# Performance work log

Hardware: AMD Instinct MI355X
Metric: run time of the kernel (lower is better)

Reference implementation:

```python
import jax, jax.numpy as jnp
import numpy as np

NUM_HEADS = 8
D_MODEL = 512
HEAD_DIM = D_MODEL // NUM_HEADS


def _conv1x1(x, W, b):
    # Conv1d(kernel_size=1): x [B, Cin, N], W [Cout, Cin], b [Cout] -> [B, Cout, N]
    return jnp.einsum('oi,bin->bon', W, x) + b[None, :, None]


def setup_inputs() -> dict:
    key = jax.random.key(0)
    ks = jax.random.split(key, 12)
    B, D, N, Mlen = 4, D_MODEL, 2048, 2048
    inp = {
        'query': jax.random.normal(ks[0], (B, D, N), dtype=jnp.float32),
        'key':   jax.random.normal(ks[1], (B, D, Mlen), dtype=jnp.float32),
        'value': jax.random.normal(ks[2], (B, D, Mlen), dtype=jnp.float32),
        'M':     jnp.ones((B, N, Mlen), dtype=jnp.int32),
    }
    scale = 0.02
    inp['Wq'] = jax.random.normal(ks[3], (D, D), dtype=jnp.float32) * scale
    inp['bq'] = jnp.zeros((D,), dtype=jnp.float32)
    inp['Wk'] = jax.random.normal(ks[4], (D, D), dtype=jnp.float32) * scale
    inp['bk'] = jnp.zeros((D,), dtype=jnp.float32)
    inp['Wv'] = jax.random.normal(ks[5], (D, D), dtype=jnp.float32) * scale
    inp['bv'] = jnp.zeros((D,), dtype=jnp.float32)
    inp['Wm'] = jax.random.normal(ks[6], (D, D), dtype=jnp.float32) * scale
    inp['bm'] = jnp.zeros((D,), dtype=jnp.float32)
    return inp


def reference(query, key, value, M, Wq, bq, Wk, bk, Wv, bv, Wm, bm):
    B = query.shape[0]
    # 1x1-conv projections, then channel split as [head_dim, heads] (matches torch .view)
    q = _conv1x1(query, Wq, bq).reshape(B, HEAD_DIM, NUM_HEADS, -1)  # [B, d, h, N]
    k = _conv1x1(key,   Wk, bk).reshape(B, HEAD_DIM, NUM_HEADS, -1)  # [B, d, h, M]
    v = _conv1x1(value, Wv, bv).reshape(B, HEAD_DIM, NUM_HEADS, -1)  # [B, d, h, M]
    scores = jnp.einsum('bdhn,bdhm->bhnm', q, k) / jnp.sqrt(jnp.float32(HEAD_DIM))
    # mask: positions with M==0 are disallowed -> fill with -finfo.max
    bad = (1 - M)[:, None, :, :].astype(bool)  # [B, 1, N, M], broadcasts over heads
    scores = jnp.where(bad, -jnp.finfo(scores.dtype).max, scores)
    prob = jax.nn.softmax(scores, axis=-1)  # [B, h, N, M]
    x = jnp.einsum('bhnm,bdhm->bdhn', prob, v)  # [B, d, h, N]
    out = _conv1x1(x.reshape(B, HEAD_DIM * NUM_HEADS, -1), Wm, bm)  # [B, D, N]
    return out
```

## Files before the change

### kernel.cpp

```cpp
#include <hip/hip_runtime.h>

typedef __attribute__((ext_vector_type(8))) short s8v;
typedef __attribute__((ext_vector_type(4))) float f4v;
typedef _Float16 h4 __attribute__((ext_vector_type(4)));
typedef unsigned short u16;
typedef unsigned long long u64;

#define DM 512
#define NH 8
#define HD 64
#define BB 4
#define NN 2048

__device__ __forceinline__ float bf2f(u16 x){ return __uint_as_float(((unsigned)x)<<16); }
__device__ __forceinline__ u16 f2bf(float f){
  unsigned u = __float_as_uint(f);
  u += 0x7FFFu + ((u>>16)&1u);
  return (u16)(u>>16);
}
__device__ __forceinline__ void gl2lds16(const u16* g, u16* l){
  __builtin_amdgcn_global_load_lds((__attribute__((address_space(1))) void*)(g),
                                   (__attribute__((address_space(3))) void*)(l), 16, 0, 0);
}

__global__ __launch_bounds__(256) void k_maskpack(const int* M, u64* bits){
  int tid = threadIdx.x;
  int wv = tid>>6, lane = tid&63;
  size_t w0 = (size_t)blockIdx.x*64 + wv*16;
  #pragma unroll
  for (int it=0; it<16; it++){
    int v = M[(w0+it)*64 + lane];
    u64 bal = __ballot(v == 1);
    if (lane == 0) bits[w0+it] = bal;
  }
}

__global__ void k_prep(const float* Wq, const float* bq, const float* Wk, const float* bk,
                       const float* Wv, const float* bv, const float* Wm,
                       u16* Wp, u16* Wmp, float* bp,
                       const u64* bits, u64* allw){
  int blk = blockIdx.x, tid = threadIdx.x;
  if (blk < 1536){
    int t = blk >> 9, op = blk & 511;
    int srow = ((op & 63) << 3) | (op >> 6);
    const float* W = (t==0) ? Wq : ((t==1) ? Wk : Wv);
    for (int j = tid; j < 512; j += 256)
      Wp[((size_t)t*512 + op)*512 + j] = f2bf(W[(size_t)srow*512 + j]);
  } else if (blk < 2048){
    int o = blk - 1536;
    for (int c = tid; c < 512; c += 256){
      int scol = ((c & 63) << 3) | (c >> 6);
      Wmp[(size_t)o*512 + c] = f2bf(Wm[(size_t)o*512 + scol]);
    }
  } else if (blk == 2048){
    for (int idx = tid; idx < 1536; idx += 256){
      int t = idx >> 9, op = idx & 511;
      const float* bs = (t==0) ? bq : ((t==1) ? bk : bv);
      int srow = ((op & 63) << 3) | (op >> 6);
      bp[idx] = bs[srow];
    }
  } else {
    __shared__ u64 red[256];
    int bnt = blk - 2049;
    int mt = tid & 31, rg = tid >> 5;
    const u64* base = bits + (size_t)bnt*64*32;
    u64 v = ~0ull;
    #pragma unroll
    for (int j=0;j<8;j++) v &= base[(size_t)(rg*8+j)*32 + mt];
    red[tid] = v;
    __syncthreads();
    if (tid < 32){
      u64 a = red[tid];
      #pragma unroll
      for (int g2=1; g2<8; g2++) a &= red[g2*32 + tid];
      allw[(size_t)bnt*32 + tid] = a;
    }
  }
}

__global__ __launch_bounds__(256) void k_transpose(const float* q, const float* k, const float* v, u16* XT){
  __shared__ u16 T[64*72];
  int blk = blockIdx.x, tid = threadIdx.x;
  int rt = blk & 31; blk >>= 5;
  int it = blk & 7;  blk >>= 3;
  int b  = blk & 3;  int t = blk >> 2;
  const float* src = (t==0) ? q : ((t==1) ? k : v);
  src += (size_t)b*DM*NN;
  int i0 = it*64, r0 = rt*64;
  int il = tid>>4, rj = (tid&15)*4;
  #pragma unroll
  for (int p=0;p<4;p++){
    int i = il + p*16;
    float4 vv = *(const float4*)&src[(size_t)(i0+i)*NN + r0 + rj];
    float fv[4] = {vv.x, vv.y, vv.z, vv.w};
    #pragma unroll
    for (int qq=0;qq<4;qq++){
      int r = rj + qq;
      int sr = ((r&3)<<4) | (r>>2);
      T[sr*72 + i] = f2bf(fv[qq]);
    }
  }
  __syncthreads();
  u16* dst = XT + ((size_t)(t*4+b)*NN)*DM;
  int rl = tid>>3, ib = (tid&7)*8;
  #pragma unroll
  for (int p=0;p<2;p++){
    int r = rl + p*32;
    int sr = ((r&3)<<4) | (r>>2);
    s8v vv = *(s8v*)&T[sr*72 + ib];
    *(s8v*)&dst[(size_t)(r0+r)*DM + i0 + ib] = vv;
  }
}

__global__ __launch_bounds__(256) void k_proj(const u16* XT, const u16* Wp, const float* bp,
                                              u16* P, u16* VT){
  __shared__ u16 Al[128*32];
  __shared__ u16 Bl[128*32];
  __shared__ u16 S[128*72];
  int blk = blockIdx.x, tid = threadIdx.x;
  int nt = blk & 3; int mt = blk >> 2;
  int tb = mt >> 4;
  int t  = tb >> 2, b = tb & 3;
  int r0 = (mt & 15)*128, o0 = nt*128;
  const u16* Abase = XT + ((size_t)tb*NN + r0)*DM;
  const u16* Bbase = Wp + ((size_t)t*512 + o0)*DM;

  int w = tid>>6, L = tid&63, li = L&15, lq = L>>4;
  int wr = w>>1, wc = w&1;
  int srow = tid>>2;
  int g8   = ((tid&3) ^ ((tid>>3)&3))*8;
  u16* AldsW = &Al[((tid&192))*8];
  u16* BldsW = &Bl[((tid&192))*8];
  int sw = (li>>1)&3;

  f4v acc[4][4];
  #pragma unroll
  for (int a=0;a<4;a++)
    #pragma unroll
    for (int c2=0;c2<4;c2++) acc[a][c2] = (f4v){0.f,0.f,0.f,0.f};

  for (int kk=0; kk<16; kk++){
    int k0 = kk*32;
    __syncthreads();
    #pragma unroll
    for (int c=0;c<2;c++){
      gl2lds16(&Abase[(size_t)(srow + c*64)*DM + k0 + g8], AldsW + c*2048);
      gl2lds16(&Bbase[(size_t)(srow + c*64)*DM + k0 + g8], BldsW + c*2048);
    }
    __syncthreads();
    s8v af[4], bfr[4];
    #pragma unroll
    for (int a=0;a<4;a++){
      int r = wr*64 + a*16 + li;
      af[a] = *(s8v*)&Al[r*32 + ((lq ^ sw))*8];
    }
    #pragma unroll
    for (int c2=0;c2<4;c2++){
      int r = wc*64 + c2*16 + li;
      bfr[c2] = *(s8v*)&Bl[r*32 + ((lq ^ sw))*8];
    }
    #pragma unroll
    for (int a=0;a<4;a++)
      #pragma unroll
      for (int c2=0;c2<4;c2++)
        acc[a][c2] = __builtin_amdgcn_mfma_f32_16x16x32_bf16(af[a], bfr[c2], acc[a][c2], 0, 0, 0);
  }

  if (t < 2){
    float scale = (t==0) ? 0.125f : 1.0f;
    #pragma unroll
    for (int p=0;p<2;p++){
      if (wc == p){
        #pragma unroll
        for (int c2=0;c2<4;c2++){
          int cl = c2*16 + li;
          float bias = bp[t*512 + o0 + p*64 + cl];
          #pragma unroll
          for (int a=0;a<4;a++)
            #pragma unroll
            for (int ri=0;ri<4;ri++)
              S[(wr*64 + a*16 + lq*4 + ri)*72 + cl] = f2bf((acc[a][c2][ri] + bias)*scale);
        }
      }
      __syncthreads();
      int row = tid>>1, cb = (tid&1)*32;
      int hh = (o0>>6) + p;
      u16* Pb = P + (((size_t)tb*NH + hh)*NN + r0 + row)*HD + cb;
      #pragma unroll
      for (int c=0;c<4;c++){
        s8v vv = *(s8v*)&S[row*72 + cb + c*8];
        *(s8v*)&Pb[c*8] = vv;
      }
      __syncthreads();
    }
  } else {
    #pragma unroll
    for (int p=0;p<2;p++){
      if (wc == p){
        #pragma unroll
        for (int c2=0;c2<4;c2++){
          int cl = c2*16 + li;
          float bias = bp[2*512 + o0 + p*64 + cl];
          #pragma unroll
          for (int a=0;a<4;a++)
            #pragma unroll
            for (int ri=0;ri<4;ri++){
              _Float16 hh = (_Float16)(acc[a][c2][ri] + bias);
              S[(wr*64 + a*16 + lq*4 + ri)*72 + cl] = *(const u16*)&hh;
            }
        }
      }
      __syncthreads();
      int hh = (o0>>6) + p;
      u16* Vb = VT + (((size_t)b*NH + hh)*NN + r0)*HD;
      #pragma unroll
      for (int it2=0; it2<4; it2++){
        int c = tid + it2*256;
        int mb = c >> 7;
        int co = c & 127;
        int d  = co >> 1;
        int m8 = (co & 1)*8;
        u16 tmp[8];
        #pragma unroll
        for (int j=0;j<8;j++) tmp[j] = S[(mb*16 + m8 + j)*72 + d];
        *(s8v*)&Vb[(size_t)mb*1024 + d*16 + m8] = *(s8v*)&tmp[0];
      }
      __syncthreads();
    }
  }
}

__global__ __launch_bounds__(256) void k_flash(const u16* Pq, const u16* VT, const u64* bits,
                                               const u64* allw, u16* Xout){
  __shared__ __align__(16) char smem[18432 + 1024];
  float* Red = (float*)smem;
  float* lsb = (float*)(smem + 18432);

  int blk = blockIdx.x, tid = threadIdx.x;
  int bh = blk & 31; int nt = blk >> 5;
  int b = bh >> 3;
  int n0 = nt*64;
  const size_t TSZ = (size_t)BB*NH*NN*HD;
  const u16* Qb = Pq + ((size_t)bh*NN + n0)*HD;
  const u16* Kb = Pq + TSZ + (size_t)bh*NN*HD;
  const u16* Vb = VT + (size_t)bh*NN*HD;
  const u64* awp = allw + ((size_t)b*32 + nt)*32;

  int w = tid>>6, L = tid&63, li = L&15, lq = L>>4;

  s8v Qf[4][2];
  #pragma unroll
  for (int j=0;j<4;j++)
    #pragma unroll
    for (int h2=0;h2<2;h2++)
      Qf[j][h2] = *(const s8v*)&Qb[(size_t)(j*16+li)*HD + h2*32 + lq*8];

  f4v O[4][4];
  #pragma unroll
  for (int j2=0;j2<4;j2++)
    #pragma unroll
    for (int j=0;j<4;j++) O[j2][j] = (f4v){0.f,0.f,0.f,0.f};
  float ls[4] = {0.f,0.f,0.f,0.f};

  const u16* Krow = Kb + (size_t)(w*16 + li)*HD + lq*8;
  const u16* Vrow = Vb + (size_t)w*1024 + li*16 + lq*4;

  s8v cK0 = *(const s8v*)&Krow[0];
  s8v cK1 = *(const s8v*)&Krow[32];
  h4 cV[4];
  #pragma unroll
  for (int j2=0;j2<4;j2++) cV[j2] = *(const h4*)&Vrow[j2*256];

  for (int mt=0; mt<32; mt++){
    size_t noff = (size_t)((mt+1)&31)*4096;
    s8v nK0 = *(const s8v*)&Krow[noff];
    s8v nK1 = *(const s8v*)&Krow[noff + 32];
    h4 nV[4];
    #pragma unroll
    for (int j2=0;j2<4;j2++) nV[j2] = *(const h4*)&Vrow[noff + j2*256];

    u64 aw = awp[mt];
    bool fast = (aw == ~0ull);

    f4v S[4];
    #pragma unroll
    for (int j=0;j<4;j++){
      f4v c = (f4v){0.f,0.f,0.f,0.f};
      c = __builtin_amdgcn_mfma_f32_16x16x32_bf16(cK0, Qf[j][0], c, 0, 0, 0);
      c = __builtin_amdgcn_mfma_f32_16x16x32_bf16(cK1, Qf[j][1], c, 0, 0, 0);
      S[j] = c;
    }

    h4 Pf[4];
    if (fast){
      #pragma unroll
      for (int j=0;j<4;j++){
        float e0 = __expf(S[j][0]), e1 = __expf(S[j][1]);
        float e2 = __expf(S[j][2]), e3 = __expf(S[j][3]);
        ls[j] += (e0+e1)+(e2+e3);
        Pf[j][0] = (_Float16)e0; Pf[j][1] = (_Float16)e1;
        Pf[j][2] = (_Float16)e2; Pf[j][3] = (_Float16)e3;
      }
    } else {
      int mbit = w*16 + lq*4;
      #pragma unroll
      for (int j=0;j<4;j++){
        u64 mw = bits[((size_t)b*NN + n0 + j*16 + li)*32 + mt];
        float e[4];
        #pragma unroll
        for (int r=0;r<4;r++){
          float ev = __expf(S[j][r]);
          e[r] = ((mw>>(mbit+r)) & 1ull) ? ev : 0.f;
          Pf[j][r] = (_Float16)e[r];
        }
        ls[j] += (e[0]+e[1])+(e[2]+e[3]);
      }
    }

    #pragma unroll
    for (int j2=0;j2<4;j2++)
      #pragma unroll
      for (int j=0;j<4;j++)
        O[j2][j] = __builtin_amdgcn_mfma_f32_16x16x16f16(cV[j2], Pf[j], O[j2][j], 0, 0, 0);

    cK0 = nK0; cK1 = nK1;
    #pragma unroll
    for (int j2=0;j2<4;j2++) cV[j2] = nV[j2];
  }

  #pragma unroll
  for (int j=0;j<4;j++){
    float r = ls[j];
    r += __shfl_xor(r, 16); r += __shfl_xor(r, 32);
    ls[j] = r;
  }
  if (lq == 0){
    #pragma unroll
    for (int j=0;j<4;j++) lsb[w*64 + j*16 + li] = ls[j];
  }
  __syncthreads();

  #pragma unroll
  for (int ph=0; ph<4; ph++){
    if (w == ph){
      #pragma unroll
      for (int j=0;j<4;j++)
        #pragma unroll
        for (int j2=0;j2<4;j2++){
          f4v* p = (f4v*)&Red[(j*16+li)*68 + j2*16 + lq*4];
          if (ph == 0) *p = O[j2][j];
          else { f4v t = *p; t += O[j2][j]; *p = t; }
        }
    }
    __syncthreads();
  }

  int n = tid>>2, d0 = (tid&3)*16;
  float s = lsb[n] + lsb[64+n] + lsb[128+n] + lsb[192+n];
  float inv = (s > 0.f) ? 1.0f/s : 0.f;
  int h = bh & 7;
  u16* Xo = Xout + ((size_t)b*NN + n0 + n)*DM + h*HD + d0;
  u16 tmp[16];
  #pragma unroll
  for (int e2=0;e2<4;e2++){
    f4v vv = *(f4v*)&Red[n*68 + d0 + e2*4];
    #pragma unroll
    for (int q2=0;q2<4;q2++) tmp[e2*4+q2] = f2bf(vv[q2]*inv);
  }
  *(s8v*)&Xo[0] = *(s8v*)&tmp[0];
  *(s8v*)&Xo[8] = *(s8v*)&tmp[8];
}

__global__ __launch_bounds__(256) void k_out(const u16* Wmp, const u16* Xout, const float* bm, float* out){
  __shared__ u16 Al[64*32];
  __shared__ u16 Bl[128*32];
  int blk = blockIdx.x, tid = threadIdx.x;
  int nt = blk & 15; blk >>= 4;
  int ot = blk & 7;  int b = blk >> 3;
  int o0 = ot*64, n0 = nt*128;
  const u16* Abase = Wmp + (size_t)o0*DM;
  const u16* Bbase = Xout + ((size_t)b*NN + n0)*DM;

  int w = tid>>6, L = tid&63, li = L&15, lq = L>>4;
  int wo = w&1, wn = w>>1;
  int srow = tid>>2;
  int g8   = ((tid&3) ^ ((tid>>3)&3))*8;
  u16* AldsW = &Al[((tid&192))*8];
  u16* BldsW = &Bl[((tid&192))*8];
  int sw = (li>>1)&3;

  f4v acc[2][4];
  #pragma unroll
  for (int a=0;a<2;a++)
    #pragma unroll
    for (int c2=0;c2<4;c2++) acc[a][c2] = (f4v){0.f,0.f,0.f,0.f};

  for (int kk=0; kk<16; kk++){
    int k0 = kk*32;
    __syncthreads();
    gl2lds16(&Abase[(size_t)srow*DM + k0 + g8], AldsW);
    #pragma unroll
    for (int c=0;c<2;c++)
      gl2lds16(&Bbase[(size_t)(srow + c*64)*DM + k0 + g8], BldsW + c*2048);
    __syncthreads();
    s8v af[2], bfr[4];
    #pragma unroll
    for (int a=0;a<2;a++){
      int r = wo*32 + a*16 + li;
      af[a] = *(s8v*)&Al[r*32 + ((lq ^ sw))*8];
    }
    #pragma unroll
    for (int c2=0;c2<4;c2++){
      int r = wn*64 + c2*16 + li;
      bfr[c2] = *(s8v*)&Bl[r*32 + ((lq ^ sw))*8];
    }
    #pragma unroll
    for (int a=0;a<2;a++)
      #pragma unroll
      for (int c2=0;c2<4;c2++)
        acc[a][c2] = __builtin_amdgcn_mfma_f32_16x16x32_bf16(af[a], bfr[c2], acc[a][c2], 0, 0, 0);
  }

  #pragma unroll
  for (int a=0;a<2;a++){
    #pragma unroll
    for (int ri=0;ri<4;ri++){
      int o = o0 + wo*32 + a*16 + lq*4 + ri;
      float bias = bm[o];
      float* ob = out + ((size_t)b*DM + o)*NN + n0 + wn*64;
      #pragma unroll
      for (int c2=0;c2<4;c2++)
        ob[c2*16 + li] = acc[a][c2][ri] + bias;
    }
  }
}

extern "C" void kernel_launch(void* const* d_in, const int* in_sizes, int n_in,
                              void* d_out, int out_size, void* d_ws, size_t ws_size,
                              hipStream_t stream){
  const float* q  = (const float*)d_in[0];
  const float* k  = (const float*)d_in[1];
  const float* v  = (const float*)d_in[2];
  const int*   M  = (const int*)d_in[3];
  const float* Wq = (const float*)d_in[4];
  const float* bq = (const float*)d_in[5];
  const float* Wk = (const float*)d_in[6];
  const float* bk = (const float*)d_in[7];
  const float* Wv = (const float*)d_in[8];
  const float* bv = (const float*)d_in[9];
  const float* Wm = (const float*)d_in[10];
  const float* bm = (const float*)d_in[11];

  char* ws = (char*)d_ws;
  u16*   XT   = (u16*)(ws + 0);
  u16*   P    = (u16*)(ws + 25165824);
  u16*   VT   = (u16*)(ws + 41943040);
  u16*   Wp   = (u16*)(ws + 50331648);
  u16*   Wmp  = (u16*)(ws + 51904512);
  float* bp   = (float*)(ws + 52428800);
  u64*   bits = (u64*)(ws + 52434944);
  u16*   Xout = (u16*)(ws + 54532096);
  u64*   allw = (u64*)(ws + 62920704);
  float* out  = (float*)d_out;

  k_maskpack<<<4096, 256, 0, stream>>>(M, bits);
  k_prep<<<2177, 256, 0, stream>>>(Wq, bq, Wk, bk, Wv, bv, Wm, Wp, Wmp, bp, bits, allw);
  k_transpose<<<3072, 256, 0, stream>>>(q, k, v, XT);
  k_proj<<<768, 256, 0, stream>>>(XT, Wp, bp, P, VT);
  k_flash<<<1024, 256, 0, stream>>>(P, VT, bits, allw, Xout);
  k_out<<<512, 256, 0, stream>>>(Wmp, Xout, bm, out);
}
```

Baseline: 277.3 us.

## Use 16x16x32 f16 MFMA for PV with repacked V layout and exp2

Processes two 64-key tiles per iteration in the flash kernel so the P·V product can use the wider 16x16x32 f16 MFMA instead of 16x16x16. The V projection output is repacked so each lane loads 8 contiguous halves per MFMA operand. The Q scale now folds in log2(e) so softmax uses native exp2. It also adds s_setprio around the MFMA blocks and reorders the projection block index mapping. V loads are no longer prefetched one iteration ahead, which may expose memory latency, and the extra score tiles raise register pressure.

```diff
diff --git a/kernel.cpp b/kernel.cpp
--- a/kernel.cpp
+++ b/kernel.cpp
@@ -2,7 +2,7 @@
 
 typedef __attribute__((ext_vector_type(8))) short s8v;
 typedef __attribute__((ext_vector_type(4))) float f4v;
-typedef _Float16 h4 __attribute__((ext_vector_type(4)));
+typedef _Float16 h8 __attribute__((ext_vector_type(8)));
 typedef unsigned short u16;
 typedef unsigned long long u64;
 
@@ -11,6 +11,9 @@
 #define HD 64
 #define BB 4
 #define NN 2048
+
+extern "C" __device__ float __ocml_native_exp2_f32(float);
+__device__ __forceinline__ float fexp2(float x){ return __ocml_native_exp2_f32(x); }
 
 __device__ __forceinline__ float bf2f(u16 x){ return __uint_as_float(((unsigned)x)<<16); }
 __device__ __forceinline__ u16 f2bf(float f){
@@ -118,7 +121,7 @@
   __shared__ u16 Bl[128*32];
   __shared__ u16 S[128*72];
   int blk = blockIdx.x, tid = threadIdx.x;
-  int nt = blk & 3; int mt = blk >> 2;
+  int nt = blk / 192; int mt = blk % 192;
   int tb = mt >> 4;
   int t  = tb >> 2, b = tb & 3;
   int r0 = (mt & 15)*128, o0 = nt*128;
@@ -167,7 +170,7 @@
   }
 
   if (t < 2){
-    float scale = (t==0) ? 0.125f : 1.0f;
+    float scale = (t==0) ? 0.18033688f : 1.0f;
     #pragma unroll
     for (int p=0;p<2;p++){
       if (wc == p){
@@ -194,6 +197,7 @@
       __syncthreads();
     }
   } else {
+    int mp = mt & 15;
     #pragma unroll
     for (int p=0;p<2;p++){
       if (wc == p){
@@ -212,18 +216,20 @@
       }
       __syncthreads();
       int hh = (o0>>6) + p;
-      u16* Vb = VT + (((size_t)b*NH + hh)*NN + r0)*HD;
+      u16* Vbw = VT + ((size_t)(b*NH + hh)*16 + mp)*8192;
       #pragma unroll
       for (int it2=0; it2<4; it2++){
         int c = tid + it2*256;
-        int mb = c >> 7;
-        int co = c & 127;
-        int d  = co >> 1;
-        int m8 = (co & 1)*8;
+        int w2  = c >> 8;
+        int d   = (c >> 2) & 63;
+        int lq2 = c & 3;
         u16 tmp[8];
         #pragma unroll
-        for (int j=0;j<8;j++) tmp[j] = S[(mb*16 + m8 + j)*72 + d];
-        *(s8v*)&Vb[(size_t)mb*1024 + d*16 + m8] = *(s8v*)&tmp[0];
+        for (int t2=0;t2<8;t2++){
+          int ml = ((t2>>2)<<6) + w2*16 + lq2*4 + (t2&3);
+          tmp[t2] = S[ml*72 + d];
+        }
+        *(s8v*)&Vbw[(size_t)w2*2048 + d*32 + lq2*8] = *(s8v*)&tmp[0];
       }
       __syncthreads();
     }
@@ -263,53 +269,56 @@
   float ls[4] = {0.f,0.f,0.f,0.f};
 
   const u16* Krow = Kb + (size_t)(w*16 + li)*HD + lq*8;
-  const u16* Vrow = Vb + (size_t)w*1024 + li*16 + lq*4;
-
-  s8v cK0 = *(const s8v*)&Krow[0];
-  s8v cK1 = *(const s8v*)&Krow[32];
-  h4 cV[4];
-  #pragma unroll
-  for (int j2=0;j2<4;j2++) cV[j2] = *(const h4*)&Vrow[j2*256];
-
-  for (int mt=0; mt<32; mt++){
-    size_t noff = (size_t)((mt+1)&31)*4096;
-    s8v nK0 = *(const s8v*)&Krow[noff];
-    s8v nK1 = *(const s8v*)&Krow[noff + 32];
-    h4 nV[4];
-    #pragma unroll
-    for (int j2=0;j2<4;j2++) nV[j2] = *(const h4*)&Vrow[noff + j2*256];
-
-    u64 aw = awp[mt];
-    bool fast = (aw == ~0ull);
-
+  const u16* Vrow = Vb + (size_t)w*2048 + li*32 + lq*8;
+
+  s8v cKA0 = *(const s8v*)&Krow[0];
+  s8v cKA1 = *(const s8v*)&Krow[32];
+  s8v cKB0 = *(const s8v*)&Krow[4096];
+  s8v cKB1 = *(const s8v*)&Krow[4128];
+
+  int mbit = w*16 + lq*4;
+
+  for (int mp=0; mp<16; mp++){
+    size_t noff = (size_t)((mp+1)&15)*8192;
+    s8v nKA0 = *(const s8v*)&Krow[noff];
+    s8v nKA1 = *(const s8v*)&Krow[noff + 32];
+    s8v nKB0 = *(const s8v*)&Krow[noff + 4096];
+    s8v nKB1 = *(const s8v*)&Krow[noff + 4128];
+    size_t voff = (size_t)mp*8192;
+    h8 cV[4];
+    #pragma unroll
+    for (int j2=0;j2<4;j2++) cV[j2] = *(const h8*)&Vrow[voff + j2*512];
+
+    u64 awA = awp[2*mp], awB = awp[2*mp+1];
+    h8 Pf[4];
     f4v S[4];
+
+    __builtin_amdgcn_s_setprio(1);
     #pragma unroll
     for (int j=0;j<4;j++){
       f4v c = (f4v){0.f,0.f,0.f,0.f};
-      c = __builtin_amdgcn_mfma_f32_16x16x32_bf16(cK0, Qf[j][0], c, 0, 0, 0);
-      c = __builtin_amdgcn_mfma_f32_16x16x32_bf16(cK1, Qf[j][1], c, 0, 0, 0);
+      c = __builtin_amdgcn_mfma_f32_16x16x32_bf16(cKA0, Qf[j][0], c, 0, 0, 0);
+      c = __builtin_amdgcn_mfma_f32_16x16x32_bf16(cKA1, Qf[j][1], c, 0, 0, 0);
       S[j] = c;
     }
-
-    h4 Pf[4];
-    if (fast){
+    __builtin_amdgcn_s_setprio(0);
+    if (awA == ~0ull){
       #pragma unroll
       for (int j=0;j<4;j++){
-        float e0 = __expf(S[j][0]), e1 = __expf(S[j][1]);
-        float e2 = __expf(S[j][2]), e3 = __expf(S[j][3]);
+        float e0 = fexp2(S[j][0]), e1 = fexp2(S[j][1]);
+        float e2 = fexp2(S[j][2]), e3 = fexp2(S[j][3]);
         ls[j] += (e0+e1)+(e2+e3);
         Pf[j][0] = (_Float16)e0; Pf[j][1] = (_Float16)e1;
         Pf[j][2] = (_Float16)e2; Pf[j][3] = (_Float16)e3;
       }
     } else {
-      int mbit = w*16 + lq*4;
       #pragma unroll
       for (int j=0;j<4;j++){
-        u64 mw = bits[((size_t)b*NN + n0 + j*16 + li)*32 + mt];
+        u64 mw = bits[((size_t)b*NN + n0 + j*16 + li)*32 + 2*mp];
         float e[4];
         #pragma unroll
         for (int r=0;r<4;r++){
-          float ev = __expf(S[j][r]);
+          float ev = fexp2(S[j][r]);
           e[r] = ((mw>>(mbit+r)) & 1ull) ? ev : 0.f;
           Pf[j][r] = (_Float16)e[r];
         }
@@ -317,15 +326,48 @@
       }
     }
 
+    __builtin_amdgcn_s_setprio(1);
+    #pragma unroll
+    for (int j=0;j<4;j++){
+      f4v c = (f4v){0.f,0.f,0.f,0.f};
+      c = __builtin_amdgcn_mfma_f32_16x16x32_bf16(cKB0, Qf[j][0], c, 0, 0, 0);
+      c = __builtin_amdgcn_mfma_f32_16x16x32_bf16(cKB1, Qf[j][1], c, 0, 0, 0);
+      S[j] = c;
+    }
+    __builtin_amdgcn_s_setprio(0);
+    if (awB == ~0ull){
+      #pragma unroll
+      for (int j=0;j<4;j++){
+        float e0 = fexp2(S[j][0]), e1 = fexp2(S[j][1]);
+        float e2 = fexp2(S[j][2]), e3 = fexp2(S[j][3]);
+        ls[j] += (e0+e1)+(e2+e3);
+        Pf[j][4] = (_Float16)e0; Pf[j][5] = (_Float16)e1;
+        Pf[j][6] = (_Float16)e2; Pf[j][7] = (_Float16)e3;
+      }
+    } else {
+      #pragma unroll
+      for (int j=0;j<4;j++){
+        u64 mw = bits[((size_t)b*NN + n0 + j*16 + li)*32 + 2*mp + 1];
+        float e[4];
+        #pragma unroll
+        for (int r=0;r<4;r++){
+          float ev = fexp2(S[j][r]);
+          e[r] = ((mw>>(mbit+r)) & 1ull) ? ev : 0.f;
+          Pf[j][4+r] = (_Float16)e[r];
+        }
+        ls[j] += (e[0]+e[1])+(e[2]+e[3]);
+      }
+    }
+
+    __builtin_amdgcn_s_setprio(1);
     #pragma unroll
     for (int j2=0;j2<4;j2++)
       #pragma unroll
       for (int j=0;j<4;j++)
-        O[j2][j] = __builtin_amdgcn_mfma_f32_16x16x16f16(cV[j2], Pf[j], O[j2][j], 0, 0, 0);
-
-    cK0 = nK0; cK1 = nK1;
-    #pragma unroll
-    for (int j2=0;j2<4;j2++) cV[j2] = nV[j2];
+        O[j2][j] = __builtin_amdgcn_mfma_f32_16x16x32_f16(cV[j2], Pf[j], O[j2][j], 0, 0, 0);
+    __builtin_amdgcn_s_setprio(0);
+
+    cKA0 = nKA0; cKA1 = nKA1; cKB0 = nKB0; cKB1 = nKB1;
   }
 
   #pragma unroll
```

Result: no change. 278.2 us (+0.3%).
